# Kernel optimization log

Hardware: AMD Instinct MI355X
Metric: run time of the kernel (lower is better)

## Reference

```python
import jax, jax.numpy as jnp
import numpy as np

P = 32    # cardinality (number of parallel paths)
C = 256   # block input/output channels
D = 4     # bottleneck width per path
EPS = 1e-3  # Keras BatchNormalization default epsilon


def setup_inputs() -> dict:
    key = jax.random.key(0)
    ks = jax.random.split(key, 24)
    def nrm(k, shape, s=0.05):
        return jax.random.normal(k, shape, dtype=jnp.float32) * s
    inp = {}
    inp["x"] = jax.random.normal(ks[0], (8, 56, 56, C), dtype=jnp.float32)
    # conv weights/biases, stacked over the path axis P
    inp["W1"] = nrm(ks[1], (P, C, D))          # 1x1 conv C->4
    inp["B1"] = nrm(ks[2], (P, D))
    inp["W2"] = nrm(ks[3], (P, 3, 3, D, D))    # 3x3 conv 4->4 (HWIO)
    inp["B2"] = nrm(ks[4], (P, D))
    inp["W3"] = nrm(ks[5], (P, D, C))          # 1x1 conv 4->256
    inp["B3"] = nrm(ks[6], (P, C))
    # BatchNorm (inference): gamma, beta, moving mean, moving var per stage
    inp["G1"]  = 1.0 + nrm(ks[7], (P, D));  inp["Be1"] = nrm(ks[8], (P, D))
    inp["M1"]  = nrm(ks[9], (P, D));        inp["V1"]  = 1.0 + 0.1 * jax.random.uniform(ks[10], (P, D), dtype=jnp.float32)
    inp["G2"]  = 1.0 + nrm(ks[11], (P, D)); inp["Be2"] = nrm(ks[12], (P, D))
    inp["M2"]  = nrm(ks[13], (P, D));       inp["V2"]  = 1.0 + 0.1 * jax.random.uniform(ks[14], (P, D), dtype=jnp.float32)
    inp["G3"]  = 1.0 + nrm(ks[15], (P, C)); inp["Be3"] = nrm(ks[16], (P, C))
    inp["M3"]  = nrm(ks[17], (P, C));       inp["V3"]  = 1.0 + 0.1 * jax.random.uniform(ks[18], (P, C), dtype=jnp.float32)
    return inp


def _bn(x, g, b, m, v):
    # inference batch-norm: affine over channel axis
    return g * (x - m) * jax.lax.rsqrt(v + EPS) + b


def _path(x, w1, b1, g1, be1, m1, v1, w2, b2, g2, be2, m2, v2, w3, b3, g3, be3, m3, v3):
    h = jnp.einsum('nhwc,cd->nhwd', x, w1) + b1            # 1x1 conv C->D
    h = jax.nn.relu(_bn(h, g1, be1, m1, v1))
    h = jax.lax.conv_general_dilated(
        h, w2, window_strides=(1, 1), padding='SAME',
        dimension_numbers=('NHWC', 'HWIO', 'NHWC')) + b2   # 3x3 conv D->D
    h = jax.nn.relu(_bn(h, g2, be2, m2, v2))
    h = jnp.einsum('nhwd,dc->nhwc', h, w3) + b3            # 1x1 conv D->C
    h = jax.nn.relu(_bn(h, g3, be3, m3, v3))
    return h  # Dropout(0.2) is identity at inference


def reference(x, W1, B1, G1, Be1, M1, V1, W2, B2, G2, Be2, M2, V2, W3, B3, G3, Be3, M3, V3):
    # vmap over the 32 cardinality paths; x is shared (in_axes=None)
    paths = jax.vmap(_path, in_axes=(None,) + (0,) * 18)(
        x, W1, B1, G1, Be1, M1, V1, W2, B2, G2, Be2, M2, V2, W3, B3, G3, Be3, M3, V3)
    return jax.nn.relu(paths.sum(axis=0) + x)
```

## Files before the change

kernel.cpp:

```cpp
#include <hip/hip_runtime.h>

#define BATCH 8
#define HH 56
#define WW 56
#define NPOS (BATCH*HH*WW)
#define C 256
#define P 32
#define D 4
#define J 128
#define EPS 1e-3f
#define H2S 136

typedef __attribute__((ext_vector_type(8))) short bf16x8_t;
typedef __attribute__((ext_vector_type(4))) float f32x4_t;

__device__ __forceinline__ unsigned short f2bf(float f) {
    union { float f; unsigned int i; } v; v.f = f;
    unsigned int r = v.i + 0x7fffu + ((v.i >> 16) & 1u);
    return (unsigned short)(r >> 16);
}
__device__ __forceinline__ uint2 pack4_trunc(float4 v) {
    uint2 r;
    r.x = __builtin_amdgcn_perm(__float_as_uint(v.y), __float_as_uint(v.x), 0x07060302u);
    r.y = __builtin_amdgcn_perm(__float_as_uint(v.w), __float_as_uint(v.z), 0x07060302u);
    return r;
}

__global__ __launch_bounds__(256) void fold_params(
    const float* __restrict__ W1, const float* __restrict__ B1,
    const float* __restrict__ W2, const float* __restrict__ B2,
    const float* __restrict__ W3, const float* __restrict__ B3,
    const float* __restrict__ G1, const float* __restrict__ Be1,
    const float* __restrict__ M1, const float* __restrict__ V1,
    const float* __restrict__ G2, const float* __restrict__ Be2,
    const float* __restrict__ M2, const float* __restrict__ V2,
    const float* __restrict__ G3, const float* __restrict__ Be3,
    const float* __restrict__ M3, const float* __restrict__ V3,
    unsigned short* __restrict__ W1bf, float* __restrict__ b1f,
    float* __restrict__ w2q, float* __restrict__ b2t,
    unsigned short* __restrict__ WB, unsigned short* __restrict__ zb)
{
    int idx = blockIdx.x * 256 + threadIdx.x;

    if (idx < C*J) {
        int j = idx >> 8, c = idx & 255;
        int p = j >> 2, d = j & 3;
        float s = G1[j] * rsqrtf(V1[j] + EPS);
        W1bf[idx] = f2bf(W1[(p*C + c)*D + d] * s);
        return;
    }
    idx -= C*J;
    if (idx < J) {
        float s = G1[idx] * rsqrtf(V1[idx] + EPS);
        b1f[idx] = B1[idx] * s + Be1[idx] - M1[idx] * s;
        return;
    }
    idx -= J;
    if (idx < 9*D*D*P) {
        int do_ = idx & 3, p = (idx >> 2) & 31;
        int r2 = idx >> 7, di = r2 & 3, k9 = r2 >> 2;
        int j = p*4 + do_;
        float s = G2[j] * rsqrtf(V2[j] + EPS);
        w2q[idx] = W2[((p*9 + k9)*4 + di)*4 + do_] * s;
        return;
    }
    idx -= 9*D*D*P;
    if (idx < J) {
        int do_ = idx >> 5, p = idx & 31;
        int j = p*4 + do_;
        float s = G2[j] * rsqrtf(V2[j] + EPS);
        b2t[idx] = B2[j] * s + Be2[j] - M2[j] * s;
        return;
    }
    idx -= J;
    if (idx < P*C*8) {
        int s8 = idx & 7;
        int c = (idx >> 3) & 255;
        int p = idx >> 11;
        float sc = G3[p*C + c] * rsqrtf(V3[p*C + c] + EPS);
        float v = 0.f;
        if (s8 < 4)       v = W3[(p*D + s8)*C + c] * sc;
        else if (s8 == 4) v = B3[p*C + c] * sc + Be3[p*C + c] - M3[p*C + c] * sc;
        WB[idx] = f2bf(v);
        return;
    }
    idx -= P*C*8;
    if (idx < 8) { zb[idx] = 0; return; }
}

__global__ __launch_bounds__(256) void fused_all(
    const float* __restrict__ x, const unsigned short* __restrict__ W1bf,
    const float* __restrict__ b1f, const float* __restrict__ w2q,
    const float* __restrict__ b2t, const unsigned short* __restrict__ WB,
    const unsigned short* __restrict__ zb, float* __restrict__ out)
{
    __shared__ unsigned short h1L[64*132];
    __shared__ unsigned short h2s[32*H2S];

    const int tid = threadIdx.x;
    int bxx = blockIdx.x;
    const int xb = bxx % 7;  bxx /= 7;
    const int yb = bxx % 14; const int b = bxx / 14;
    const int wid = tid >> 6, l = tid & 63, l15 = l & 15, quad = l >> 4;
    const int j0w = wid * 32;

    union bu { uint4 u; bf16x8_t v; };
    bu aw[2][8];
#pragma unroll
    for (int jf = 0; jf < 2; ++jf) {
        int row = j0w + jf*16 + l15;
#pragma unroll
        for (int kc = 0; kc < 8; ++kc)
            aw[jf][kc].u = *(const uint4*)&W1bf[row*C + kc*32 + quad*8];
    }

#pragma unroll
    for (int mt = 0; mt < 4; ++mt) {
        const int row = mt*16 + l15;
        int hy = (row * 205) >> 11;
        int hx = row - hy*10;
        int gy = yb*4 + hy - 1, gx = xb*8 + hx - 1;
        const bool valid = (row < 60) & (gy >= 0) & (gy < HH) & (gx >= 0) & (gx < WW);
        const unsigned mask = valid ? 0xFFFFFFFFu : 0u;
        const size_t n = valid ? (size_t)((b*HH + gy)*WW + gx) : (size_t)0;
        const float* xp = &x[n*C + quad*8];

        f32x4_t acc0 = (f32x4_t){0.f,0.f,0.f,0.f};
        f32x4_t acc1 = (f32x4_t){0.f,0.f,0.f,0.f};
#pragma unroll
        for (int kc = 0; kc < 8; ++kc) {
            float4 v0 = *(const float4*)(xp + kc*32);
            float4 v1 = *(const float4*)(xp + kc*32 + 4);
            uint2 p0 = pack4_trunc(v0), p1 = pack4_trunc(v1);
            union { uint4 u; bf16x8_t v; } bb;
            bb.u.x = p0.x; bb.u.y = p0.y; bb.u.z = p1.x; bb.u.w = p1.y;
            acc0 = __builtin_amdgcn_mfma_f32_16x16x32_bf16(aw[0][kc].v, bb.v, acc0, 0, 0, 0);
            acc1 = __builtin_amdgcn_mfma_f32_16x16x32_bf16(aw[1][kc].v, bb.v, acc1, 0, 0, 0);
        }
#pragma unroll
        for (int jf = 0; jf < 2; ++jf) {
            const f32x4_t a = jf ? acc1 : acc0;
            int jb = j0w + jf*16 + quad*4;
            float4 bias = *(const float4*)&b1f[jb];
            float v0 = fmaxf(a[0] + bias.x, 0.f);
            float v1 = fmaxf(a[1] + bias.y, 0.f);
            float v2 = fmaxf(a[2] + bias.z, 0.f);
            float v3 = fmaxf(a[3] + bias.w, 0.f);
            uint2 o;
            o.x = ((unsigned int)f2bf(v0) | ((unsigned int)f2bf(v1) << 16)) & mask;
            o.y = ((unsigned int)f2bf(v2) | ((unsigned int)f2bf(v3) << 16)) & mask;
            *(uint2*)&h1L[row*132 + jb] = o;
        }
    }
    __syncthreads();

    const int p = tid & 31;
    const int slot = tid >> 5;
    float acc[4][4];
    {
        float b0 = b2t[p], b1 = b2t[32+p], b2 = b2t[64+p], b3 = b2t[96+p];
#pragma unroll
        for (int i = 0; i < 4; ++i) {
            acc[i][0] = b0; acc[i][1] = b1; acc[i][2] = b2; acc[i][3] = b3;
        }
    }
#pragma unroll
    for (int ky = 0; ky < 3; ++ky) {
#pragma unroll
        for (int kx = 0; kx < 3; ++kx) {
            const float* wp = &w2q[(ky*3 + kx) * 512 + p*4];
            float4 w0 = *(const float4*)&wp[0];
            float4 w1 = *(const float4*)&wp[128];
            float4 w2v = *(const float4*)&wp[256];
            float4 w3v = *(const float4*)&wp[384];
#pragma unroll
            for (int i = 0; i < 4; ++i) {
                int nl = slot + i*8;
                int hp = ((nl >> 3) + ky)*10 + (nl & 7) + kx;
                uint2 hv = *(const uint2*)&h1L[hp*132 + p*4];
                float f0 = __uint_as_float(hv.x << 16);
                float f1 = __uint_as_float(hv.x & 0xffff0000u);
                float f2 = __uint_as_float(hv.y << 16);
                float f3 = __uint_as_float(hv.y & 0xffff0000u);
                acc[i][0] = fmaf(f0, w0.x, acc[i][0]);  acc[i][1] = fmaf(f0, w0.y, acc[i][1]);
                acc[i][2] = fmaf(f0, w0.z, acc[i][2]);  acc[i][3] = fmaf(f0, w0.w, acc[i][3]);
                acc[i][0] = fmaf(f1, w1.x, acc[i][0]);  acc[i][1] = fmaf(f1, w1.y, acc[i][1]);
                acc[i][2] = fmaf(f1, w1.z, acc[i][2]);  acc[i][3] = fmaf(f1, w1.w, acc[i][3]);
                acc[i][0] = fmaf(f2, w2v.x, acc[i][0]); acc[i][1] = fmaf(f2, w2v.y, acc[i][1]);
                acc[i][2] = fmaf(f2, w2v.z, acc[i][2]); acc[i][3] = fmaf(f2, w2v.w, acc[i][3]);
                acc[i][0] = fmaf(f3, w3v.x, acc[i][0]); acc[i][1] = fmaf(f3, w3v.y, acc[i][1]);
                acc[i][2] = fmaf(f3, w3v.z, acc[i][2]); acc[i][3] = fmaf(f3, w3v.w, acc[i][3]);
            }
        }
    }
#pragma unroll
    for (int i = 0; i < 4; ++i) {
        int nl = slot + i*8;
        uint2 o;
        o.x = (unsigned int)f2bf(fmaxf(acc[i][0], 0.f)) |
              ((unsigned int)f2bf(fmaxf(acc[i][1], 0.f)) << 16);
        o.y = (unsigned int)f2bf(fmaxf(acc[i][2], 0.f)) |
              ((unsigned int)f2bf(fmaxf(acc[i][3], 0.f)) << 16);
        *(uint2*)&h2s[nl*H2S + p*4] = o;
    }
    __syncthreads();

    const int cb = wid * 64;
    const unsigned short* wbp;
    int pstr, cstr;
    if (quad == 0) {
        wbp = &WB[((size_t)(cb + l15)) * 8];
        pstr = C * 8;
        cstr = 16 * 8;
    } else {
        wbp = zb;
        pstr = 0; cstr = 0;
    }

    const f32x4_t zero = (f32x4_t){0.f, 0.f, 0.f, 0.f};
    f32x4_t dacc[2][4];
#pragma unroll
    for (int ps = 0; ps < 2; ++ps)
#pragma unroll
        for (int ct = 0; ct < 4; ++ct) dacc[ps][ct] = zero;
    const unsigned int one = 0x3f80u;

#pragma unroll 2
    for (int pp = 0; pp < 16; ++pp) {
        uint4 h0 = *(const uint4*)&h2s[l15*H2S + pp*8];
        uint4 h1 = *(const uint4*)&h2s[(16 + l15)*H2S + pp*8];
        union au { unsigned int u[4]; bf16x8_t v; };
        au A00, A01, A10, A11;
        A00.u[0] = h0.x; A00.u[1] = h0.y; A00.u[2] = one; A00.u[3] = 0u;
        A01.u[0] = h0.z; A01.u[1] = h0.w; A01.u[2] = one; A01.u[3] = 0u;
        A10.u[0] = h1.x; A10.u[1] = h1.y; A10.u[2] = one; A10.u[3] = 0u;
        A11.u[0] = h1.z; A11.u[1] = h1.w; A11.u[2] = one; A11.u[3] = 0u;
        const unsigned short* pb0 = wbp + pp*2*pstr;
        const unsigned short* pb1 = pb0 + pstr;
#pragma unroll
        for (int ct = 0; ct < 4; ++ct) {
            union bu2 { uint4 u; bf16x8_t v; } B0, B1;
            B0.u = *(const uint4*)(pb0 + ct*cstr);
            B1.u = *(const uint4*)(pb1 + ct*cstr);
            f32x4_t z00 = __builtin_amdgcn_mfma_f32_16x16x32_bf16(A00.v, B0.v, zero, 0, 0, 0);
            f32x4_t z01 = __builtin_amdgcn_mfma_f32_16x16x32_bf16(A01.v, B1.v, zero, 0, 0, 0);
            f32x4_t z10 = __builtin_amdgcn_mfma_f32_16x16x32_bf16(A10.v, B0.v, zero, 0, 0, 0);
            f32x4_t z11 = __builtin_amdgcn_mfma_f32_16x16x32_bf16(A11.v, B1.v, zero, 0, 0, 0);
#pragma unroll
            for (int r = 0; r < 4; ++r) {
                dacc[0][ct][r] += fmaxf(z00[r], 0.f) + fmaxf(z01[r], 0.f);
                dacc[1][ct][r] += fmaxf(z10[r], 0.f) + fmaxf(z11[r], 0.f);
            }
        }
    }

#pragma unroll
    for (int ps = 0; ps < 2; ++ps) {
#pragma unroll
        for (int r = 0; r < 4; ++r) {
            int nl = ps*16 + quad*4 + r;
            int gy = yb*4 + (nl >> 3), gx = xb*8 + (nl & 7);
            size_t n = (size_t)((b*HH + gy)*WW + gx);
            const float* xr = &x[n*C + cb + l15];
            float* orow = &out[n*C + cb + l15];
#pragma unroll
            for (int ct = 0; ct < 4; ++ct) {
                float v = dacc[ps][ct][r] + xr[ct*16];
                orow[ct*16] = fmaxf(v, 0.f);
            }
        }
    }
}

extern "C" void kernel_launch(void* const* d_in, const int* in_sizes, int n_in,
                              void* d_out, int out_size, void* d_ws, size_t ws_size,
                              hipStream_t stream) {
    const float* x  = (const float*)d_in[0];
    const float* W1 = (const float*)d_in[1];
    const float* B1 = (const float*)d_in[2];
    const float* W2 = (const float*)d_in[3];
    const float* B2 = (const float*)d_in[4];
    const float* W3 = (const float*)d_in[5];
    const float* B3 = (const float*)d_in[6];
    const float* G1 = (const float*)d_in[7];
    const float* Be1= (const float*)d_in[8];
    const float* M1 = (const float*)d_in[9];
    const float* V1 = (const float*)d_in[10];
    const float* G2 = (const float*)d_in[11];
    const float* Be2= (const float*)d_in[12];
    const float* M2 = (const float*)d_in[13];
    const float* V2 = (const float*)d_in[14];
    const float* G3 = (const float*)d_in[15];
    const float* Be3= (const float*)d_in[16];
    const float* M3 = (const float*)d_in[17];
    const float* V3 = (const float*)d_in[18];

    char* wsb = (char*)d_ws;
    unsigned short* W1bf = (unsigned short*)(wsb + 0);
    unsigned short* WB   = (unsigned short*)(wsb + 65536);
    float*          w2q  = (float*)(wsb + 196608);
    float*          b1f  = (float*)(wsb + 215040);
    float*          b2t  = (float*)(wsb + 215552);
    unsigned short* zb   = (unsigned short*)(wsb + 216064);

    const int fold_tasks = C*J + J + 9*D*D*P + J + P*C*8 + 8;
    fold_params<<<(fold_tasks + 255)/256, 256, 0, stream>>>(
        W1, B1, W2, B2, W3, B3, G1, Be1, M1, V1, G2, Be2, M2, V2,
        G3, Be3, M3, V3, W1bf, b1f, w2q, b2t, WB, zb);

    fused_all<<<8*14*7, 256, 0, stream>>>(x, W1bf, b1f, w2q, b2t, WB, zb,
                                          (float*)d_out);
}
```

Measured before the change: 197.5 us.

## Shrink spatial tile to 4x4 and stage bf16 input halo in LDS

Output tiles shrink from 4x8 to 4x4 positions, which doubles the grid to 1568 blocks. The 6x6 input halo is loaded once, converted to bf16 and stored in swizzled LDS, and the first 1x1 conv MFMAs then read their operands from LDS instead of global memory. LDS is aliased so h2s reuses the input staging area, which needs an extra barrier. Halo overhead rises (36 positions computed for 16 outputs instead of 60 for 32), but more blocks and lower per-block register and LDS pressure are meant to raise occupancy and load balance.

```diff
diff --git a/kernel.cpp b/kernel.cpp
--- a/kernel.cpp
+++ b/kernel.cpp
@@ -94,73 +94,85 @@
     const float* __restrict__ b2t, const unsigned short* __restrict__ WB,
     const unsigned short* __restrict__ zb, float* __restrict__ out)
 {
-    __shared__ unsigned short h1L[64*132];
-    __shared__ unsigned short h2s[32*H2S];
+    __shared__ unsigned short smem[36*256 + 36*132];
+    unsigned short* xs  = smem;
+    unsigned short* h1L = smem + 36*256;
+    unsigned short* h2s = smem;
 
     const int tid = threadIdx.x;
     int bxx = blockIdx.x;
-    const int xb = bxx % 7;  bxx /= 7;
-    const int yb = bxx % 14; const int b = bxx / 14;
+    const int xb = bxx % 14;  bxx /= 14;
+    const int yb = bxx % 14;  const int b = bxx / 14;
     const int wid = tid >> 6, l = tid & 63, l15 = l & 15, quad = l >> 4;
     const int j0w = wid * 32;
 
+#pragma unroll
+    for (int it = 0; it < 5; ++it) {
+        int idx = it*256 + tid;
+        int pos = idx >> 5, g = idx & 31;
+        if (pos < 36) {
+            int hy = (pos*43) >> 8, hx = pos - hy*6;
+            int gy = yb*4 + hy - 1, gx = xb*4 + hx - 1;
+            uint4 st; st.x = 0u; st.y = 0u; st.z = 0u; st.w = 0u;
+            if (gy >= 0 && gy < HH && gx >= 0 && gx < WW) {
+                const float* xp = &x[(size_t)((b*HH + gy)*WW + gx) * C + g*8];
+                float4 v0 = *(const float4*)xp;
+                float4 v1 = *(const float4*)(xp + 4);
+                uint2 p0 = pack4_trunc(v0), p1 = pack4_trunc(v1);
+                st.x = p0.x; st.y = p0.y; st.z = p1.x; st.w = p1.y;
+            }
+            *(uint4*)&xs[pos*256 + ((g ^ (pos & 7)) * 8)] = st;
+        }
+    }
+    __syncthreads();
+
     union bu { uint4 u; bf16x8_t v; };
-    bu aw[2][8];
 #pragma unroll
     for (int jf = 0; jf < 2; ++jf) {
-        int row = j0w + jf*16 + l15;
+        bu aw[8];
+        const int wrow = j0w + jf*16 + l15;
 #pragma unroll
         for (int kc = 0; kc < 8; ++kc)
-            aw[jf][kc].u = *(const uint4*)&W1bf[row*C + kc*32 + quad*8];
-    }
-
-#pragma unroll
-    for (int mt = 0; mt < 4; ++mt) {
-        const int row = mt*16 + l15;
-        int hy = (row * 205) >> 11;
-        int hx = row - hy*10;
-        int gy = yb*4 + hy - 1, gx = xb*8 + hx - 1;
-        const bool valid = (row < 60) & (gy >= 0) & (gy < HH) & (gx >= 0) & (gx < WW);
-        const unsigned mask = valid ? 0xFFFFFFFFu : 0u;
-        const size_t n = valid ? (size_t)((b*HH + gy)*WW + gx) : (size_t)0;
-        const float* xp = &x[n*C + quad*8];
-
-        f32x4_t acc0 = (f32x4_t){0.f,0.f,0.f,0.f};
-        f32x4_t acc1 = (f32x4_t){0.f,0.f,0.f,0.f};
-#pragma unroll
-        for (int kc = 0; kc < 8; ++kc) {
-            float4 v0 = *(const float4*)(xp + kc*32);
-            float4 v1 = *(const float4*)(xp + kc*32 + 4);
-            uint2 p0 = pack4_trunc(v0), p1 = pack4_trunc(v1);
-            union { uint4 u; bf16x8_t v; } bb;
-            bb.u.x = p0.x; bb.u.y = p0.y; bb.u.z = p1.x; bb.u.w = p1.y;
-            acc0 = __builtin_amdgcn_mfma_f32_16x16x32_bf16(aw[0][kc].v, bb.v, acc0, 0, 0, 0);
-            acc1 = __builtin_amdgcn_mfma_f32_16x16x32_bf16(aw[1][kc].v, bb.v, acc1, 0, 0, 0);
-        }
-#pragma unroll
-        for (int jf = 0; jf < 2; ++jf) {
-            const f32x4_t a = jf ? acc1 : acc0;
-            int jb = j0w + jf*16 + quad*4;
-            float4 bias = *(const float4*)&b1f[jb];
-            float v0 = fmaxf(a[0] + bias.x, 0.f);
-            float v1 = fmaxf(a[1] + bias.y, 0.f);
-            float v2 = fmaxf(a[2] + bias.z, 0.f);
-            float v3 = fmaxf(a[3] + bias.w, 0.f);
-            uint2 o;
-            o.x = ((unsigned int)f2bf(v0) | ((unsigned int)f2bf(v1) << 16)) & mask;
-            o.y = ((unsigned int)f2bf(v2) | ((unsigned int)f2bf(v3) << 16)) & mask;
-            *(uint2*)&h1L[row*132 + jb] = o;
+            aw[kc].u = *(const uint4*)&W1bf[wrow*C + kc*32 + quad*8];
+#pragma unroll
+        for (int mt = 0; mt < 3; ++mt) {
+            const int row = mt*16 + l15;
+            const int rrow = (row < 36) ? row : 0;
+            int hy = (row*43) >> 8;
+            int hx = row - hy*6;
+            int gy = yb*4 + hy - 1, gx = xb*4 + hx - 1;
+            const bool valid = (row < 36) & (gy >= 0) & (gy < HH) & (gx >= 0) & (gx < WW);
+            const unsigned mask = valid ? 0xFFFFFFFFu : 0u;
+            f32x4_t acc = (f32x4_t){0.f,0.f,0.f,0.f};
+#pragma unroll
+            for (int kc = 0; kc < 8; ++kc) {
+                int g = (kc*4 + quad) ^ (rrow & 7);
+                bf16x8_t bb = *(const bf16x8_t*)&xs[rrow*256 + g*8];
+                acc = __builtin_amdgcn_mfma_f32_16x16x32_bf16(aw[kc].v, bb, acc, 0, 0, 0);
+            }
+            if (row < 36) {
+                int jb = j0w + jf*16 + quad*4;
+                float4 bias = *(const float4*)&b1f[jb];
+                float v0 = fmaxf(acc[0] + bias.x, 0.f);
+                float v1 = fmaxf(acc[1] + bias.y, 0.f);
+                float v2 = fmaxf(acc[2] + bias.z, 0.f);
+                float v3 = fmaxf(acc[3] + bias.w, 0.f);
+                uint2 o;
+                o.x = ((unsigned int)f2bf(v0) | ((unsigned int)f2bf(v1) << 16)) & mask;
+                o.y = ((unsigned int)f2bf(v2) | ((unsigned int)f2bf(v3) << 16)) & mask;
+                *(uint2*)&h1L[row*132 + jb] = o;
+            }
         }
     }
     __syncthreads();
 
     const int p = tid & 31;
     const int slot = tid >> 5;
-    float acc[4][4];
+    float acc[2][4];
     {
         float b0 = b2t[p], b1 = b2t[32+p], b2 = b2t[64+p], b3 = b2t[96+p];
 #pragma unroll
-        for (int i = 0; i < 4; ++i) {
+        for (int i = 0; i < 2; ++i) {
             acc[i][0] = b0; acc[i][1] = b1; acc[i][2] = b2; acc[i][3] = b3;
         }
     }
@@ -174,9 +186,9 @@
             float4 w2v = *(const float4*)&wp[256];
             float4 w3v = *(const float4*)&wp[384];
 #pragma unroll
-            for (int i = 0; i < 4; ++i) {
+            for (int i = 0; i < 2; ++i) {
                 int nl = slot + i*8;
-                int hp = ((nl >> 3) + ky)*10 + (nl & 7) + kx;
+                int hp = ((nl >> 2) + ky)*6 + (nl & 3) + kx;
                 uint2 hv = *(const uint2*)&h1L[hp*132 + p*4];
                 float f0 = __uint_as_float(hv.x << 16);
                 float f1 = __uint_as_float(hv.x & 0xffff0000u);
@@ -193,8 +205,9 @@
             }
         }
     }
-#pragma unroll
-    for (int i = 0; i < 4; ++i) {
+    __syncthreads();
+#pragma unroll
+    for (int i = 0; i < 2; ++i) {
         int nl = slot + i*8;
         uint2 o;
         o.x = (unsigned int)f2bf(fmaxf(acc[i][0], 0.f)) |
@@ -218,23 +231,18 @@
     }
 
     const f32x4_t zero = (f32x4_t){0.f, 0.f, 0.f, 0.f};
-    f32x4_t dacc[2][4];
-#pragma unroll
-    for (int ps = 0; ps < 2; ++ps)
-#pragma unroll
-        for (int ct = 0; ct < 4; ++ct) dacc[ps][ct] = zero;
+    f32x4_t dacc[4];
+#pragma unroll
+    for (int ct = 0; ct < 4; ++ct) dacc[ct] = zero;
     const unsigned int one = 0x3f80u;
 
 #pragma unroll 2
     for (int pp = 0; pp < 16; ++pp) {
         uint4 h0 = *(const uint4*)&h2s[l15*H2S + pp*8];
-        uint4 h1 = *(const uint4*)&h2s[(16 + l15)*H2S + pp*8];
         union au { unsigned int u[4]; bf16x8_t v; };
-        au A00, A01, A10, A11;
-        A00.u[0] = h0.x; A00.u[1] = h0.y; A00.u[2] = one; A00.u[3] = 0u;
-        A01.u[0] = h0.z; A01.u[1] = h0.w; A01.u[2] = one; A01.u[3] = 0u;
-        A10.u[0] = h1.x; A10.u[1] = h1.y; A10.u[2] = one; A10.u[3] = 0u;
-        A11.u[0] = h1.z; A11.u[1] = h1.w; A11.u[2] = one; A11.u[3] = 0u;
+        au A0, A1;
+        A0.u[0] = h0.x; A0.u[1] = h0.y; A0.u[2] = one; A0.u[3] = 0u;
+        A1.u[0] = h0.z; A1.u[1] = h0.w; A1.u[2] = one; A1.u[3] = 0u;
         const unsigned short* pb0 = wbp + pp*2*pstr;
         const unsigned short* pb1 = pb0 + pstr;
 #pragma unroll
@@ -242,32 +250,25 @@
             union bu2 { uint4 u; bf16x8_t v; } B0, B1;
             B0.u = *(const uint4*)(pb0 + ct*cstr);
             B1.u = *(const uint4*)(pb1 + ct*cstr);
-            f32x4_t z00 = __builtin_amdgcn_mfma_f32_16x16x32_bf16(A00.v, B0.v, zero, 0, 0, 0);
-            f32x4_t z01 = __builtin_amdgcn_mfma_f32_16x16x32_bf16(A01.v, B1.v, zero, 0, 0, 0);
-            f32x4_t z10 = __builtin_amdgcn_mfma_f32_16x16x32_bf16(A10.v, B0.v, zero, 0, 0, 0);
-            f32x4_t z11 = __builtin_amdgcn_mfma_f32_16x16x32_bf16(A11.v, B1.v, zero, 0, 0, 0);
-#pragma unroll
-            for (int r = 0; r < 4; ++r) {
-                dacc[0][ct][r] += fmaxf(z00[r], 0.f) + fmaxf(z01[r], 0.f);
-                dacc[1][ct][r] += fmaxf(z10[r], 0.f) + fmaxf(z11[r], 0.f);
-            }
-        }
-    }
-
-#pragma unroll
-    for (int ps = 0; ps < 2; ++ps) {
-#pragma unroll
-        for (int r = 0; r < 4; ++r) {
-            int nl = ps*16 + quad*4 + r;
-            int gy = yb*4 + (nl >> 3), gx = xb*8 + (nl & 7);
-            size_t n = (size_t)((b*HH + gy)*WW + gx);
-            const float* xr = &x[n*C + cb + l15];
-            float* orow = &out[n*C + cb + l15];
-#pragma unroll
-            for (int ct = 0; ct < 4; ++ct) {
-                float v = dacc[ps][ct][r] + xr[ct*16];
-                orow[ct*16] = fmaxf(v, 0.f);
-            }
+            f32x4_t z0 = __builtin_amdgcn_mfma_f32_16x16x32_bf16(A0.v, B0.v, zero, 0, 0, 0);
+            f32x4_t z1 = __builtin_amdgcn_mfma_f32_16x16x32_bf16(A1.v, B1.v, zero, 0, 0, 0);
+#pragma unroll
+            for (int r = 0; r < 4; ++r)
+                dacc[ct][r] += fmaxf(z0[r], 0.f) + fmaxf(z1[r], 0.f);
+        }
+    }
+
+#pragma unroll
+    for (int r = 0; r < 4; ++r) {
+        int nl = quad*4 + r;
+        int gy = yb*4 + (nl >> 2), gx = xb*4 + (nl & 3);
+        size_t n = (size_t)((b*HH + gy)*WW + gx);
+        const float* xr = &x[n*C + cb + l15];
+        float* orow = &out[n*C + cb + l15];
+#pragma unroll
+        for (int ct = 0; ct < 4; ++ct) {
+            float v = dacc[ct][r] + xr[ct*16];
+            orow[ct*16] = fmaxf(v, 0.f);
         }
     }
 }
@@ -308,6 +309,6 @@
         W1, B1, W2, B2, W3, B3, G1, Be1, M1, V1, G2, Be2, M2, V2,
         G3, Be3, M3, V3, W1bf, b1f, w2q, b2t, WB, zb);
 
-    fused_all<<<8*14*7, 256, 0, stream>>>(x, W1bf, b1f, w2q, b2t, WB, zb,
-                                          (float*)d_out);
-}
+    fused_all<<<8*14*14, 256, 0, stream>>>(x, W1bf, b1f, w2q, b2t, WB, zb,
+                                           (float*)d_out);
+}
```

Measured after the change: 188.5 us. 4.6% less time.
